# Performance work log

Measured on AMD Instinct MI355X. Metric: run time of the kernel, lower is better.

Reference implementation:

```python
import jax, jax.numpy as jnp
import numpy as np
from jax import lax

IMG = 28  # MNIST side
KH = KW = 3  # conv kernel size


def setup_inputs() -> dict:
    key = jax.random.key(0)
    ks = jax.random.split(key, 4)
    B = 65536
    return {
        "x": jax.random.normal(ks[0], (B, 784), dtype=jnp.float32),
        "conv_w": jax.random.normal(ks[1], (KH, KW), dtype=jnp.float32),
        "w1": jax.random.normal(ks[2], (676, 300), dtype=jnp.float32),
        "b1": jnp.zeros((1, 300), dtype=jnp.float32),
        "w2": jax.random.normal(ks[3], (300, 10), dtype=jnp.float32),
        "b2": jnp.zeros((1, 10), dtype=jnp.float32),
    }


def reference(x, conv_w, w1, b1, w2, b2):
    B = x.shape[0]
    img = x.reshape(B, 1, IMG, IMG)  # NCHW, single channel
    # Valid 2D cross-correlation (matches the per-pixel tensordot in Convolve)
    kern = conv_w.reshape(1, 1, KH, KW)  # OIHW
    conv = lax.conv_general_dilated(
        img, kern, window_strides=(1, 1), padding="VALID",
        dimension_numbers=("NCHW", "OIHW", "NCHW"))  # [B,1,26,26]
    feat = conv.reshape(B, (IMG - KH + 1) * (IMG - KW + 1))  # [B,676]
    a1 = jax.nn.relu(feat @ w1 + b1)
    return a1 @ w2 + b2
```

## Files before the change

kernel.cpp:

```cpp
#include <hip/hip_runtime.h>
#include <stdint.h>

#define IMG 28
#define OD 26
#define K_REAL 784
#define N_REAL 300
#define KPAD 800
#define NPAD 320
#define NT 20
#define NKS 25
#define KS2N 10
#define BM 64
#define THREADS 256

typedef float f32x4 __attribute__((ext_vector_type(4)));
typedef short s16x8 __attribute__((ext_vector_type(8)));

__device__ __forceinline__ unsigned short f2bf(float f) {
  union { float f; uint32_t u; } v; v.f = f;
  uint32_t u = v.u;
  return (unsigned short)((u + 0x7fffu + ((u >> 16) & 1u)) >> 16);
}

__global__ void pack_weff(const float* __restrict__ conv_w,
                          const float* __restrict__ w1,
                          unsigned short* __restrict__ weffp) {
  int t = blockIdx.x * blockDim.x + threadIdx.x;
  if (t >= KPAD * NPAD) return;
  int i = t / NPAD;
  int j = t - i * NPAD;
  float v = 0.f;
  if (i < K_REAL && j < N_REAL) {
    int r = i / IMG, c = i % IMG;
#pragma unroll
    for (int kh = 0; kh < 3; ++kh) {
      int orr = r - kh;
      if (orr < 0 || orr >= OD) continue;
#pragma unroll
      for (int kw = 0; kw < 3; ++kw) {
        int occ = c - kw;
        if (occ < 0 || occ >= OD) continue;
        v += conv_w[kh * 3 + kw] * w1[(orr * OD + occ) * N_REAL + j];
      }
    }
  }
  int ks = i >> 5, i5 = i & 31, g = i5 >> 3, jj = i5 & 7;
  int nt = j >> 4, c16 = j & 15;
  int lane = g * 16 + c16;
  weffp[(((size_t)ks * NT + nt) * 64 + lane) * 8 + jj] = f2bf(v);
}

__global__ void pack_w2(const float* __restrict__ w2,
                        unsigned short* __restrict__ w2p) {
  int t = blockIdx.x * blockDim.x + threadIdx.x;
  if (t >= 320 * 16) return;
  int k = t >> 4, j = t & 15;
  float v = (k < N_REAL && j < 10) ? w2[k * 10 + j] : 0.f;
  int ks = k >> 5, g = (k & 31) >> 3, jj = k & 7;
  w2p[((size_t)ks * 64 + g * 16 + j) * 8 + jj] = f2bf(v);
}

__global__ void __launch_bounds__(THREADS)
fused_kernel(const float* __restrict__ x,
             const float* __restrict__ b1,
             const float* __restrict__ b2,
             const unsigned short* __restrict__ weffp,
             const unsigned short* __restrict__ w2p,
             float* __restrict__ out) {
  __shared__ uint4 ldsbuf[41984 / 16];
  unsigned char* lds = (unsigned char*)ldsbuf;

  const int tid = threadIdx.x;
  const int wid = tid >> 6;
  const int lane = tid & 63;
  const int g = lane >> 4;
  const int c16 = lane & 15;
  const long row0 = (long)blockIdx.x * BM + wid * 16;

  const float* xrow = x + (size_t)(row0 + c16) * K_REAL + g * 8;

  f32x4 acc[NT];
#pragma unroll
  for (int i = 0; i < NT; ++i) acc[i] = f32x4{0.f, 0.f, 0.f, 0.f};

#define STAGE(ks_, sel_)                                                        \
  {                                                                             \
    _Pragma("unroll")                                                           \
    for (int i_ = 0; i_ < 5; ++i_) {                                            \
      int ci_ = wid * 5 + i_;                                                   \
      const unsigned char* gsrc_ = (const unsigned char*)weffp +                \
          (size_t)(ks_) * 20480 + ci_ * 1024 + lane * 16;                       \
      __builtin_amdgcn_global_load_lds(                                         \
          (const __attribute__((address_space(1))) uint32_t*)gsrc_,             \
          (__attribute__((address_space(3))) uint32_t*)&lds[(sel_) * 20480 + ci_ * 1024], \
          16, 0, 0);                                                            \
    }                                                                           \
  }

  STAGE(0, 0);
  __syncthreads();

#pragma unroll 1
  for (int ks = 0; ks < NKS - 1; ++ks) {
    STAGE(ks + 1, (ks + 1) & 1);
    f32x4 a0 = *(const f32x4*)(xrow + ks * 32);
    f32x4 a1v = *(const f32x4*)(xrow + ks * 32 + 4);
    s16x8 af;
#pragma unroll
    for (int j = 0; j < 4; ++j) {
      af[j] = (short)f2bf(a0[j]);
      af[j + 4] = (short)f2bf(a1v[j]);
    }
    const unsigned char* bufc = &lds[(ks & 1) * 20480];
#pragma unroll
    for (int nt = 0; nt < NT; ++nt) {
      s16x8 bfr = *(const s16x8*)(bufc + nt * 1024 + lane * 16);
      acc[nt] = __builtin_amdgcn_mfma_f32_16x16x32_bf16(af, bfr, acc[nt], 0, 0, 0);
    }
    __syncthreads();
  }
  {
    s16x8 af = s16x8{0, 0, 0, 0, 0, 0, 0, 0};
    if (g < 2) {
      f32x4 a0 = *(const f32x4*)(xrow + 24 * 32);
      f32x4 a1v = *(const f32x4*)(xrow + 24 * 32 + 4);
#pragma unroll
      for (int j = 0; j < 4; ++j) {
        af[j] = (short)f2bf(a0[j]);
        af[j + 4] = (short)f2bf(a1v[j]);
      }
    }
    const unsigned char* bufc = &lds[0];
#pragma unroll
    for (int nt = 0; nt < NT; ++nt) {
      s16x8 bfr = *(const s16x8*)(bufc + nt * 1024 + lane * 16);
      acc[nt] = __builtin_amdgcn_mfma_f32_16x16x32_bf16(af, bfr, acc[nt], 0, 0, 0);
    }
  }
  __syncthreads();

  unsigned short* a1w = (unsigned short*)(void*)&lds[wid * 10496];
  const int rbase = g * 4;
#pragma unroll
  for (int nt = 0; nt < NT; ++nt) {
    int col = nt * 16 + c16;
    float bias = (col < N_REAL) ? b1[col] : 0.f;
#pragma unroll
    for (int r = 0; r < 4; ++r) {
      float v = acc[nt][r] + bias;
      v = v > 0.f ? v : 0.f;
      a1w[(rbase + r) * 328 + col] = f2bf(v);
    }
  }
  __syncthreads();

  f32x4 acc2 = f32x4{0.f, 0.f, 0.f, 0.f};
#pragma unroll
  for (int ks2 = 0; ks2 < KS2N; ++ks2) {
    s16x8 a2 = *(const s16x8*)((const unsigned char*)a1w + c16 * 656 + ks2 * 64 + g * 16);
    s16x8 b2f = *(const s16x8*)(w2p + ((size_t)ks2 * 64 + lane) * 8);
    acc2 = __builtin_amdgcn_mfma_f32_16x16x32_bf16(a2, b2f, acc2, 0, 0, 0);
  }
  if (c16 < 10) {
    float bv = b2[c16];
#pragma unroll
    for (int r = 0; r < 4; ++r) {
      long grow = row0 + rbase + r;
      out[grow * 10 + c16] = acc2[r] + bv;
    }
  }
}

extern "C" void kernel_launch(void* const* d_in, const int* in_sizes, int n_in,
                              void* d_out, int out_size, void* d_ws, size_t ws_size,
                              hipStream_t stream) {
  const float* x      = (const float*)d_in[0];
  const float* conv_w = (const float*)d_in[1];
  const float* w1     = (const float*)d_in[2];
  const float* b1     = (const float*)d_in[3];
  const float* w2     = (const float*)d_in[4];
  const float* b2     = (const float*)d_in[5];
  float* out = (float*)d_out;
  const int B = in_sizes[0] / K_REAL;

  unsigned short* weffp = (unsigned short*)d_ws;
  unsigned short* w2p   = (unsigned short*)((char*)d_ws + 512000);

  pack_weff<<<(KPAD * NPAD + 255) / 256, 256, 0, stream>>>(conv_w, w1, weffp);
  pack_w2<<<(320 * 16 + 255) / 256, 256, 0, stream>>>(w2, w2p);
  fused_kernel<<<B / BM, THREADS, 0, stream>>>(x, b1, b2, weffp, w2p, out);
}
```

Before: 332.7 us.

## Load B fragments directly from global memory instead of LDS staging

Drops the double-buffered global_load_lds staging of packed weight tiles and the per-step block barriers. Each wave now reads its B fragments straight from global memory, relying on L1/L2 caching. LDS now holds only the per-wave a1 tile, so block-wide syncs are removed. The cost is that all four waves fetch the same weights separately through the cache with no shared staging, and there is no longer an explicit prefetch overlapping loads with MFMA work.

```diff
diff --git a/kernel.cpp b/kernel.cpp
--- a/kernel.cpp
+++ b/kernel.cpp
@@ -67,8 +67,7 @@
              const unsigned short* __restrict__ weffp,
              const unsigned short* __restrict__ w2p,
              float* __restrict__ out) {
-  __shared__ uint4 ldsbuf[41984 / 16];
-  unsigned char* lds = (unsigned char*)ldsbuf;
+  __shared__ unsigned short a1lds[4 * 16 * 328];
 
   const int tid = threadIdx.x;
   const int wid = tid >> 6;
@@ -78,31 +77,14 @@
   const long row0 = (long)blockIdx.x * BM + wid * 16;
 
   const float* xrow = x + (size_t)(row0 + c16) * K_REAL + g * 8;
+  const s16x8* bfrag = (const s16x8*)weffp + lane;
 
   f32x4 acc[NT];
 #pragma unroll
   for (int i = 0; i < NT; ++i) acc[i] = f32x4{0.f, 0.f, 0.f, 0.f};
 
-#define STAGE(ks_, sel_)                                                        \
-  {                                                                             \
-    _Pragma("unroll")                                                           \
-    for (int i_ = 0; i_ < 5; ++i_) {                                            \
-      int ci_ = wid * 5 + i_;                                                   \
-      const unsigned char* gsrc_ = (const unsigned char*)weffp +                \
-          (size_t)(ks_) * 20480 + ci_ * 1024 + lane * 16;                       \
-      __builtin_amdgcn_global_load_lds(                                         \
-          (const __attribute__((address_space(1))) uint32_t*)gsrc_,             \
-          (__attribute__((address_space(3))) uint32_t*)&lds[(sel_) * 20480 + ci_ * 1024], \
-          16, 0, 0);                                                            \
-    }                                                                           \
-  }
-
-  STAGE(0, 0);
-  __syncthreads();
-
 #pragma unroll 1
   for (int ks = 0; ks < NKS - 1; ++ks) {
-    STAGE(ks + 1, (ks + 1) & 1);
     f32x4 a0 = *(const f32x4*)(xrow + ks * 32);
     f32x4 a1v = *(const f32x4*)(xrow + ks * 32 + 4);
     s16x8 af;
@@ -111,13 +93,12 @@
       af[j] = (short)f2bf(a0[j]);
       af[j + 4] = (short)f2bf(a1v[j]);
     }
-    const unsigned char* bufc = &lds[(ks & 1) * 20480];
+    const s16x8* bp = bfrag + (size_t)ks * 1280;
 #pragma unroll
     for (int nt = 0; nt < NT; ++nt) {
-      s16x8 bfr = *(const s16x8*)(bufc + nt * 1024 + lane * 16);
+      s16x8 bfr = bp[nt * 64];
       acc[nt] = __builtin_amdgcn_mfma_f32_16x16x32_bf16(af, bfr, acc[nt], 0, 0, 0);
     }
-    __syncthreads();
   }
   {
     s16x8 af = s16x8{0, 0, 0, 0, 0, 0, 0, 0};
@@ -130,16 +111,15 @@
         af[j + 4] = (short)f2bf(a1v[j]);
       }
     }
-    const unsigned char* bufc = &lds[0];
+    const s16x8* bp = bfrag + (size_t)24 * 1280;
 #pragma unroll
     for (int nt = 0; nt < NT; ++nt) {
-      s16x8 bfr = *(const s16x8*)(bufc + nt * 1024 + lane * 16);
+      s16x8 bfr = bp[nt * 64];
       acc[nt] = __builtin_amdgcn_mfma_f32_16x16x32_bf16(af, bfr, acc[nt], 0, 0, 0);
     }
   }
-  __syncthreads();
 
-  unsigned short* a1w = (unsigned short*)(void*)&lds[wid * 10496];
+  unsigned short* a1w = &a1lds[wid * 16 * 328];
   const int rbase = g * 4;
 #pragma unroll
   for (int nt = 0; nt < NT; ++nt) {
@@ -152,7 +132,6 @@
       a1w[(rbase + r) * 328 + col] = f2bf(v);
     }
   }
-  __syncthreads();
 
   f32x4 acc2 = f32x4{0.f, 0.f, 0.f, 0.f};
 #pragma unroll
```

After: 374.4 us. +12.5%, slower.

## Compute two 16-row tiles per wave and prefetch activations a step ahead

Applied to the files above, without the earlier changes.

Doubles the block row tile to 128, so each wave keeps two accumulator sets and reuses every LDS weight fragment for two MFMAs. The next K-step's x values are loaded into registers while the current step computes. bf16 conversion now uses packed v_cvt_pk_bf16_f32 instructions, and the barrier is moved to the top of the loop. This halves LDS weight traffic per MFMA and hides global-load latency, at the cost of doubled accumulator registers, fewer blocks in the grid, and a two-pass per-wave epilogue.

```diff
diff --git a/kernel.cpp b/kernel.cpp
--- a/kernel.cpp
+++ b/kernel.cpp
@@ -10,7 +10,7 @@
 #define NT 20
 #define NKS 25
 #define KS2N 10
-#define BM 64
+#define BM 128
 #define THREADS 256
 
 typedef float f32x4 __attribute__((ext_vector_type(4)));
@@ -20,6 +20,15 @@
   union { float f; uint32_t u; } v; v.f = f;
   uint32_t u = v.u;
   return (unsigned short)((u + 0x7fffu + ((u >> 16) & 1u)) >> 16);
+}
+
+__device__ __forceinline__ s16x8 cvt8(f32x4 a, f32x4 b) {
+  union { uint32_t u[4]; s16x8 v; } r;
+  asm("v_cvt_pk_bf16_f32 %0, %1, %2" : "=v"(r.u[0]) : "v"(a[0]), "v"(a[1]));
+  asm("v_cvt_pk_bf16_f32 %0, %1, %2" : "=v"(r.u[1]) : "v"(a[2]), "v"(a[3]));
+  asm("v_cvt_pk_bf16_f32 %0, %1, %2" : "=v"(r.u[2]) : "v"(b[0]), "v"(b[1]));
+  asm("v_cvt_pk_bf16_f32 %0, %1, %2" : "=v"(r.u[3]) : "v"(b[2]), "v"(b[3]));
+  return r.v;
 }
 
 __global__ void pack_weff(const float* __restrict__ conv_w,
@@ -60,81 +69,87 @@
   w2p[((size_t)ks * 64 + g * 16 + j) * 8 + jj] = f2bf(v);
 }
 
-__global__ void __launch_bounds__(THREADS)
+__global__ void __launch_bounds__(THREADS, 2)
 fused_kernel(const float* __restrict__ x,
              const float* __restrict__ b1,
              const float* __restrict__ b2,
              const unsigned short* __restrict__ weffp,
              const unsigned short* __restrict__ w2p,
              float* __restrict__ out) {
-  __shared__ uint4 ldsbuf[41984 / 16];
-  unsigned char* lds = (unsigned char*)ldsbuf;
+  __shared__ uint4 ldsq[41984 / 16];
+  unsigned char* lds = (unsigned char*)ldsq;
 
   const int tid = threadIdx.x;
   const int wid = tid >> 6;
   const int lane = tid & 63;
   const int g = lane >> 4;
   const int c16 = lane & 15;
-  const long row0 = (long)blockIdx.x * BM + wid * 16;
-
-  const float* xrow = x + (size_t)(row0 + c16) * K_REAL + g * 8;
-
-  f32x4 acc[NT];
-#pragma unroll
-  for (int i = 0; i < NT; ++i) acc[i] = f32x4{0.f, 0.f, 0.f, 0.f};
+  const long row0w = (long)blockIdx.x * BM + wid * 32;
+
+  const float* xb0 = x + (size_t)(row0w + c16) * K_REAL + g * 8;
+  const float* xb1 = xb0 + (size_t)16 * K_REAL;
+
+  f32x4 acc0[NT], acc1[NT];
+#pragma unroll
+  for (int i = 0; i < NT; ++i) {
+    acc0[i] = f32x4{0.f, 0.f, 0.f, 0.f};
+    acc1[i] = f32x4{0.f, 0.f, 0.f, 0.f};
+  }
 
 #define STAGE(ks_, sel_)                                                        \
   {                                                                             \
     _Pragma("unroll")                                                           \
     for (int i_ = 0; i_ < 5; ++i_) {                                            \
-      int ci_ = wid * 5 + i_;                                                   \
+      int off_ = i_ * 4096 + tid * 16;                                          \
       const unsigned char* gsrc_ = (const unsigned char*)weffp +                \
-          (size_t)(ks_) * 20480 + ci_ * 1024 + lane * 16;                       \
+          (size_t)(ks_) * 20480 + off_;                                         \
       __builtin_amdgcn_global_load_lds(                                         \
           (const __attribute__((address_space(1))) uint32_t*)gsrc_,             \
-          (__attribute__((address_space(3))) uint32_t*)&lds[(sel_) * 20480 + ci_ * 1024], \
+          (__attribute__((address_space(3))) uint32_t*)&lds[(sel_) * 20480 + off_], \
           16, 0, 0);                                                            \
     }                                                                           \
   }
 
   STAGE(0, 0);
-  __syncthreads();
+  f32x4 ar00 = *(const f32x4*)(xb0);
+  f32x4 ar01 = *(const f32x4*)(xb0 + 4);
+  f32x4 ar10 = *(const f32x4*)(xb1);
+  f32x4 ar11 = *(const f32x4*)(xb1 + 4);
 
 #pragma unroll 1
   for (int ks = 0; ks < NKS - 1; ++ks) {
+    __syncthreads();
+    s16x8 af0 = cvt8(ar00, ar01);
+    s16x8 af1 = cvt8(ar10, ar11);
     STAGE(ks + 1, (ks + 1) & 1);
-    f32x4 a0 = *(const f32x4*)(xrow + ks * 32);
-    f32x4 a1v = *(const f32x4*)(xrow + ks * 32 + 4);
-    s16x8 af;
-#pragma unroll
-    for (int j = 0; j < 4; ++j) {
-      af[j] = (short)f2bf(a0[j]);
-      af[j + 4] = (short)f2bf(a1v[j]);
+    if (ks < NKS - 2 || g < 2) {
+      ar00 = *(const f32x4*)(xb0 + (ks + 1) * 32);
+      ar01 = *(const f32x4*)(xb0 + (ks + 1) * 32 + 4);
+      ar10 = *(const f32x4*)(xb1 + (ks + 1) * 32);
+      ar11 = *(const f32x4*)(xb1 + (ks + 1) * 32 + 4);
     }
     const unsigned char* bufc = &lds[(ks & 1) * 20480];
 #pragma unroll
     for (int nt = 0; nt < NT; ++nt) {
       s16x8 bfr = *(const s16x8*)(bufc + nt * 1024 + lane * 16);
-      acc[nt] = __builtin_amdgcn_mfma_f32_16x16x32_bf16(af, bfr, acc[nt], 0, 0, 0);
-    }
+      acc0[nt] = __builtin_amdgcn_mfma_f32_16x16x32_bf16(af0, bfr, acc0[nt], 0, 0, 0);
+      acc1[nt] = __builtin_amdgcn_mfma_f32_16x16x32_bf16(af1, bfr, acc1[nt], 0, 0, 0);
+    }
+  }
+  {
     __syncthreads();
-  }
-  {
-    s16x8 af = s16x8{0, 0, 0, 0, 0, 0, 0, 0};
+    s16x8 af0 = s16x8{0, 0, 0, 0, 0, 0, 0, 0};
+    s16x8 af1 = s16x8{0, 0, 0, 0, 0, 0, 0, 0};
     if (g < 2) {
-      f32x4 a0 = *(const f32x4*)(xrow + 24 * 32);
-      f32x4 a1v = *(const f32x4*)(xrow + 24 * 32 + 4);
-#pragma unroll
-      for (int j = 0; j < 4; ++j) {
-        af[j] = (short)f2bf(a0[j]);
-        af[j + 4] = (short)f2bf(a1v[j]);
-      }
+      af0 = cvt8(ar00, ar01);
+      af1 = cvt8(ar10, ar11);
     }
     const unsigned char* bufc = &lds[0];
 #pragma unroll
     for (int nt = 0; nt < NT; ++nt) {
       s16x8 bfr = *(const s16x8*)(bufc + nt * 1024 + lane * 16);
-      acc[nt] = __builtin_amdgcn_mfma_f32_16x16x32_bf16(af, bfr, acc[nt], 0, 0, 0);
+      acc0[nt] = __builtin_amdgcn_mfma_f32_16x16x32_bf16(af0, bfr, acc0[nt], 0, 0, 0);
+      acc1[nt] = __builtin_amdgcn_mfma_f32_16x16x32_bf16(af1, bfr, acc1[nt], 0, 0, 0);
     }
   }
   __syncthreads();
@@ -142,31 +157,33 @@
   unsigned short* a1w = (unsigned short*)(void*)&lds[wid * 10496];
   const int rbase = g * 4;
 #pragma unroll
-  for (int nt = 0; nt < NT; ++nt) {
-    int col = nt * 16 + c16;
-    float bias = (col < N_REAL) ? b1[col] : 0.f;
-#pragma unroll
-    for (int r = 0; r < 4; ++r) {
-      float v = acc[nt][r] + bias;
-      v = v > 0.f ? v : 0.f;
-      a1w[(rbase + r) * 328 + col] = f2bf(v);
-    }
-  }
-  __syncthreads();
-
-  f32x4 acc2 = f32x4{0.f, 0.f, 0.f, 0.f};
-#pragma unroll
-  for (int ks2 = 0; ks2 < KS2N; ++ks2) {
-    s16x8 a2 = *(const s16x8*)((const unsigned char*)a1w + c16 * 656 + ks2 * 64 + g * 16);
-    s16x8 b2f = *(const s16x8*)(w2p + ((size_t)ks2 * 64 + lane) * 8);
-    acc2 = __builtin_amdgcn_mfma_f32_16x16x32_bf16(a2, b2f, acc2, 0, 0, 0);
-  }
-  if (c16 < 10) {
-    float bv = b2[c16];
-#pragma unroll
-    for (int r = 0; r < 4; ++r) {
-      long grow = row0 + rbase + r;
-      out[grow * 10 + c16] = acc2[r] + bv;
+  for (int s = 0; s < 2; ++s) {
+    const f32x4* accS = (s == 0) ? acc0 : acc1;
+#pragma unroll
+    for (int nt = 0; nt < NT; ++nt) {
+      int col = nt * 16 + c16;
+      float bias = (col < N_REAL) ? b1[col] : 0.f;
+#pragma unroll
+      for (int r = 0; r < 4; ++r) {
+        float v = accS[nt][r] + bias;
+        v = v > 0.f ? v : 0.f;
+        a1w[(rbase + r) * 328 + col] = f2bf(v);
+      }
+    }
+    f32x4 acc2 = f32x4{0.f, 0.f, 0.f, 0.f};
+#pragma unroll
+    for (int ks2 = 0; ks2 < KS2N; ++ks2) {
+      s16x8 a2 = *(const s16x8*)((const unsigned char*)a1w + c16 * 656 + ks2 * 64 + g * 16);
+      s16x8 b2f = *(const s16x8*)(w2p + ((size_t)ks2 * 64 + lane) * 8);
+      acc2 = __builtin_amdgcn_mfma_f32_16x16x32_bf16(a2, b2f, acc2, 0, 0, 0);
+    }
+    if (c16 < 10) {
+      float bv = b2[c16];
+#pragma unroll
+      for (int r = 0; r < 4; ++r) {
+        long grow = row0w + s * 16 + rbase + r;
+        out[grow * 10 + c16] = acc2[r] + bv;
+      }
     }
   }
 }
```

After: 304.6 us. 1.09x faster.
